# Optimization experiments

Hardware: AMD Instinct MI355X
Metric: run time of the kernel (lower is better)

## Reference

```python
import jax, jax.numpy as jnp
import numpy as np

LN_EPS = 1e-5
KERNEL_EPS = 1e-6


def setup_inputs() -> dict:
    key = jax.random.key(0)
    kx, kw, kb = jax.random.split(key, 3)
    B, N, D, H = 8, 2048, 256, 4
    x = jax.random.normal(kx, (B, N, D), dtype=jnp.float32) * 0.05
    log_sigmas = jnp.zeros((H, 1, 1), dtype=jnp.float32)
    W = jax.random.normal(kw, (D, D), dtype=jnp.float32) * 0.05  # torch Linear weight (out, in)
    b = jax.random.normal(kb, (D,), dtype=jnp.float32) * 0.05
    gamma = jnp.ones((D,), dtype=jnp.float32)
    beta = jnp.zeros((D,), dtype=jnp.float32)
    return {"x": x, "log_sigmas": log_sigmas, "W": W, "b": b, "gamma": gamma, "beta": beta}


def _layer_norm(y, gamma, beta):
    mu = jnp.mean(y, axis=-1, keepdims=True)
    var = jnp.var(y, axis=-1, keepdims=True)
    return (y - mu) * jax.lax.rsqrt(var + LN_EPS) * gamma + beta


def reference(x, log_sigmas, W, b, gamma, beta):
    # pairwise squared euclidean distances: (B, N, N)
    sq = jnp.sum(x * x, axis=-1)
    dist_sq = sq[:, :, None] + sq[:, None, :] - 2.0 * jnp.einsum('bnd,bmd->bnm', x, x)
    dist_sq = jnp.maximum(dist_sq, 0.0)
    # per-head Gaussian kernel adjacency, mean over heads
    sigmas = jnp.exp(log_sigmas)                      # (H,1,1)
    denom = 2.0 * sigmas ** 2 + KERNEL_EPS            # (H,1,1)
    adjs = jnp.exp(-dist_sq[:, None] / denom[None])   # (B,H,N,N)
    adj_final = jnp.mean(adjs, axis=1)                # (B,N,N)
    # aggregate, project, activate, residual layernorm
    out = jnp.einsum('bnm,bmd->bnd', adj_final, x)
    out = out @ W.T + b
    res = _layer_norm(jax.nn.elu(out) + x, gamma, beta)
    return res
```

## Files before the change

### kernel.cpp

```cpp
#include <hip/hip_runtime.h>

typedef unsigned short u16;
typedef __attribute__((ext_vector_type(8))) short bf16x8;
typedef __attribute__((ext_vector_type(4))) float f32x4;
typedef __attribute__((ext_vector_type(8))) unsigned short u16x8;

#define DEVI static __device__ __forceinline__

constexpr int Bb = 8, Nn = 2048, Dd = 256;

DEVI u16 f2bf(float f) {
    unsigned int u = __builtin_bit_cast(unsigned int, f);
    u = (u + 0x7fffu + ((u >> 16) & 1u)) >> 16;
    return (u16)u;
}
DEVI float bf2f(u16 v) {
    return __builtin_bit_cast(float, (unsigned int)v << 16);
}

DEVI void gl_lds16(const void* g, void* l) {
    __builtin_amdgcn_global_load_lds(
        (const __attribute__((address_space(1))) unsigned int*)g,
        (__attribute__((address_space(3))) unsigned int*)l, 16, 0, 0);
}

__global__ __launch_bounds__(256) void prep_xt_kernel(
    const float* __restrict__ x, u16* __restrict__ xb, u16* __restrict__ xbt,
    float* __restrict__ sq) {
    int n0 = blockIdx.x * 64;
    int b = blockIdx.y;
    int t = threadIdx.x;
    __shared__ __align__(16) u16 tile[64 * 256];
    int row = t >> 2;
    int c0 = (t & 3) * 64;
    const float* xr = x + ((size_t)(b * Nn + n0 + row)) * Dd + c0;
    u16* xbr = xb + ((size_t)(b * Nn + n0 + row)) * Dd + c0;
    float ss = 0.f;
#pragma unroll
    for (int cc = 0; cc < 16; ++cc) {
        float4 v = *(const float4*)(xr + cc * 4);
        ss += v.x * v.x + v.y * v.y + v.z * v.z + v.w * v.w;
        ushort4 o;
        o.x = f2bf(v.x); o.y = f2bf(v.y); o.z = f2bf(v.z); o.w = f2bf(v.w);
        *(ushort4*)(xbr + cc * 4) = o;
        int cb = (c0 + cc * 4) * 2;
        *(ushort4*)((char*)tile + row * 512 + (cb ^ ((row & 7) << 4))) = o;
    }
    ss += __shfl_xor(ss, 1);
    ss += __shfl_xor(ss, 2);
    if ((t & 3) == 0) sq[b * Nn + n0 + row] = ss;
    __syncthreads();
#pragma unroll
    for (int p = 0; p < 8; ++p) {
        int d = p * 32 + (t >> 3);
        int n8 = (t & 7) * 8;
        u16x8 vv;
#pragma unroll
        for (int e = 0; e < 8; ++e) {
            int r2 = n8 + e;
            vv[e] = *(const u16*)((char*)tile + r2 * 512 + ((d * 2) ^ ((r2 & 7) << 4)));
        }
        *(u16x8*)(xbt + ((size_t)(b * Dd + d)) * Nn + n0 + n8) = vv;
    }
}

__global__ void prep_w_kernel(const float* __restrict__ W, u16* __restrict__ Wb) {
    int i = (blockIdx.x * 256 + threadIdx.x) * 4;
    const float4 v = *(const float4*)(W + i);
    ushort4 o;
    o.x = f2bf(v.x); o.y = f2bf(v.y); o.z = f2bf(v.z); o.w = f2bf(v.w);
    *(ushort4*)(Wb + i) = o;
}

__global__ __launch_bounds__(256, 1) void fused_adj_kernel(
    const u16* __restrict__ xb, const u16* __restrict__ xbt,
    const float* __restrict__ sq, const float* __restrict__ lsig,
    u16* __restrict__ opart) {
    int bid = blockIdx.x;
    int xcd = bid & 7, j = bid >> 3;
    int g = xcd + 8 * (j >> 3);
    int nt8 = j & 7;
    int b = g >> 2, q = g & 3;
    int r0 = b * Nn + nt8 * 256;
    int m0b = b * Nn + q * 512;
    int mq0 = q * 512;

    int tid = threadIdx.x;
    int w = tid >> 6, l = tid & 63;
    int l15 = l & 15, lhi = l >> 4;

    __shared__ __align__(16) char smem[83968];
    char* sXmA = smem;
    char* sXmB = smem + 16384;
    char* sXmtA = smem + 32768;
    char* sXmtB = smem + 49152;
    char* sP = smem + 65536 + w * 4096;
    float* sq_lds = (float*)(smem + 81920);

    float nc[4];
#pragma unroll
    for (int h = 0; h < 4; ++h) {
        float denom = 2.f * expf(2.f * lsig[h]) + 1e-6f;
        nc[h] = -1.44269504f / denom;
    }
    bool uniform = (lsig[0] == lsig[1]) && (lsig[1] == lsig[2]) && (lsig[2] == lsig[3]);

    {
        int i2 = tid * 2;
        float2 v = *(const float2*)(sq + m0b + i2);
        *(float2*)(sq_lds + i2) = v;
    }

    bf16x8 bf[4][8];
    float sqn[4];
#pragma unroll
    for (int rg = 0; rg < 4; ++rg) {
        const u16* xr = xb + (size_t)(r0 + w * 64 + rg * 16 + l15) * Dd;
#pragma unroll
        for (int kt = 0; kt < 8; ++kt) bf[rg][kt] = *(const bf16x8*)(xr + kt * 32 + lhi * 8);
        sqn[rg] = sq[r0 + w * 64 + rg * 16 + l15];
    }

    f32x4 of[4][16];
#pragma unroll
    for (int rg = 0; rg < 4; ++rg)
#pragma unroll
        for (int dt = 0; dt < 16; ++dt) of[rg][dt] = (f32x4){0.f, 0.f, 0.f, 0.f};

    int swz = (l15 & 7) << 4;

#define STAGE(SXM, SXMT, tt) {                                                 \
    int m0_ = m0b + (tt) * 32;                                                 \
    int mc0_ = mq0 + (tt) * 32;                                                \
    _Pragma("unroll") for (int it = 0; it < 4; ++it) {                         \
        int c = w * 4 + it;                                                    \
        int row = c * 2 + (l >> 5);                                            \
        int col = l & 31;                                                      \
        gl_lds16(xb + (size_t)(m0_ + row) * Dd + (col ^ (row & 7)) * 8,        \
                 (SXM) + c * 1024);                                            \
    }                                                                           \
    _Pragma("unroll") for (int it = 0; it < 4; ++it) {                         \
        int c = w * 4 + it;                                                    \
        int drow = c * 16 + (l >> 2);                                          \
        gl_lds16(xbt + (size_t)(b * Dd + drow) * Nn + mc0_ + (l & 3) * 8,      \
                 (SXMT) + c * 1024);                                           \
    } }

#define COMPUTE(SXM, SXMT, tt) {                                               \
    _Pragma("unroll") for (int mt = 0; mt < 2; ++mt) {                         \
        float4 smv = *(const float4*)(sq_lds + (tt) * 32 + mt * 16 + lhi * 4); \
        f32x4 sfv[4];                                                          \
        _Pragma("unroll") for (int rg = 0; rg < 4; ++rg)                       \
            sfv[rg] = (f32x4){0.f, 0.f, 0.f, 0.f};                             \
        _Pragma("unroll") for (int kt = 0; kt < 8; ++kt) {                     \
            bf16x8 av = *(const bf16x8*)((SXM) + (mt * 16 + l15) * 512 +       \
                                         ((kt * 64 + lhi * 16) ^ swz));        \
            _Pragma("unroll") for (int rg = 0; rg < 4; ++rg)                   \
                sfv[rg] = __builtin_amdgcn_mfma_f32_16x16x32_bf16(             \
                    av, bf[rg][kt], sfv[rg], 0, 0, 0);                         \
        }                                                                       \
        float sm[4] = {smv.x, smv.y, smv.z, smv.w};                            \
        _Pragma("unroll") for (int rg = 0; rg < 4; ++rg) {                     \
            ushort4 pk;                                                        \
            _Pragma("unroll") for (int r = 0; r < 4; ++r) {                    \
                float d2 = fmaxf(fmaf(-2.f, sfv[rg][r], sqn[rg] + sm[r]), 0.f);\
                float p = exp2f(d2 * nc[0]);                                   \
                if (!uniform)                                                  \
                    p = 0.25f * (p + exp2f(d2 * nc[1]) + exp2f(d2 * nc[2]) +   \
                                 exp2f(d2 * nc[3]));                           \
                ((u16*)&pk)[r] = f2bf(p);                                      \
            }                                                                   \
            *(ushort4*)(sP + (rg * 16 + l15) * 64 + mt * 32 + lhi * 8) = pk;   \
        }                                                                       \
    }                                                                           \
    bf16x8 pa[4];                                                              \
    _Pragma("unroll") for (int rg = 0; rg < 4; ++rg)                           \
        pa[rg] = *(const bf16x8*)(sP + (rg * 16 + l15) * 64 + lhi * 16);       \
    _Pragma("unroll") for (int dt = 0; dt < 16; ++dt) {                        \
        bf16x8 bv = *(const bf16x8*)((SXMT) + (dt * 16 + l15) * 64 + lhi * 16);\
        _Pragma("unroll") for (int rg = 0; rg < 4; ++rg)                       \
            of[rg][dt] = __builtin_amdgcn_mfma_f32_16x16x32_bf16(              \
                pa[rg], bv, of[rg][dt], 0, 0, 0);                              \
    } }

    STAGE(sXmA, sXmtA, 0)
    __syncthreads();

    for (int tt = 0; tt < 8; ++tt) {
        int t0 = tt * 2;
        STAGE(sXmB, sXmtB, t0 + 1)
        asm volatile("s_waitcnt vmcnt(8)" ::: "memory");
        __builtin_amdgcn_s_barrier();
        COMPUTE(sXmA, sXmtA, t0)
        __builtin_amdgcn_s_barrier();
        if (tt < 7) {
            STAGE(sXmA, sXmtA, t0 + 2)
            asm volatile("s_waitcnt vmcnt(8)" ::: "memory");
        } else {
            asm volatile("s_waitcnt vmcnt(0)" ::: "memory");
        }
        __builtin_amdgcn_s_barrier();
        COMPUTE(sXmB, sXmtB, t0 + 1)
        __builtin_amdgcn_s_barrier();
    }

#undef STAGE
#undef COMPUTE

    u16* od = opart + (size_t)q * ((size_t)Bb * Nn * Dd);
#pragma unroll
    for (int rg = 0; rg < 4; ++rg)
#pragma unroll
        for (int dt = 0; dt < 16; ++dt)
#pragma unroll
            for (int r = 0; r < 4; ++r) {
                size_t row = (size_t)(r0 + w * 64 + rg * 16 + lhi * 4 + r);
                od[row * Dd + dt * 16 + l15] = f2bf(of[rg][dt][r]);
            }
}

__global__ __launch_bounds__(512, 1) void proj_ln_kernel(
    const u16* __restrict__ opart, const u16* __restrict__ Wb,
    const u16* __restrict__ xbres, const float* __restrict__ bvec,
    const float* __restrict__ gamma, const float* __restrict__ beta,
    float* __restrict__ out) {
    int tid = threadIdx.x, w = tid >> 6, l = tid & 63;
    int rg = w & 3, h = w >> 2;
    int lrow = l & 15, lhi = l >> 4;
    size_t row0 = (size_t)blockIdx.x * 64 + rg * 16;
    const size_t QS = (size_t)Bb * Nn * Dd;

    __shared__ __align__(16) float xch[8 * 16 * 2 * 64];

    f32x4 acc[16];
#pragma unroll
    for (int jt = 0; jt < 16; ++jt) acc[jt] = (f32x4){0.f, 0.f, 0.f, 0.f};

#pragma unroll
    for (int kk = 0; kk < 4; ++kk) {
        int kc = h * 4 + kk;
        float as[8] = {0.f, 0.f, 0.f, 0.f, 0.f, 0.f, 0.f, 0.f};
#pragma unroll
        for (int qq = 0; qq < 4; ++qq) {
            u16x8 v = *(const u16x8*)(opart + QS * qq + (row0 + lrow) * Dd + kc * 32 + lhi * 8);
#pragma unroll
            for (int e = 0; e < 8; ++e) as[e] += bf2f(v[e]);
        }
        bf16x8 a;
#pragma unroll
        for (int e = 0; e < 8; ++e) a[e] = (short)f2bf(as[e]);
#pragma unroll
        for (int jt = 0; jt < 16; ++jt) {
            bf16x8 bv = *(const bf16x8*)(Wb + (size_t)(jt * 16 + lrow) * Dd + kc * 32 + lhi * 8);
            acc[jt] = __builtin_amdgcn_mfma_f32_16x16x32_bf16(a, bv, acc[jt], 0, 0, 0);
        }
    }

#pragma unroll
    for (int jt = 0; jt < 16; ++jt)
#pragma unroll
        for (int qq = 0; qq < 2; ++qq) {
            int r = (1 - h) * 2 + qq;
            xch[(w * 16 + jt) * 128 + qq * 64 + l] = acc[jt][r];
        }
    __syncthreads();
#pragma unroll
    for (int jt = 0; jt < 16; ++jt)
#pragma unroll
        for (int qq = 0; qq < 2; ++qq)
            acc[jt][h * 2 + qq] += xch[((w ^ 4) * 16 + jt) * 128 + qq * 64 + l];

#pragma unroll
    for (int qq = 0; qq < 2; ++qq) {
        int r = h * 2 + qq;
        size_t grow = row0 + lhi * 4 + r;
        float vbuf[16];
        float s1 = 0.f, s2 = 0.f;
#pragma unroll
        for (int jt = 0; jt < 16; ++jt) {
            int jcol = jt * 16 + lrow;
            float v = acc[jt][r] + bvec[jcol];
            float e = v > 0.f ? v : (exp2f(v * 1.44269504f) - 1.f);
            float res = e + bf2f(xbres[grow * Dd + jcol]);
            vbuf[jt] = res;
            s1 += res;
            s2 += res * res;
        }
#pragma unroll
        for (int m = 1; m < 16; m <<= 1) {
            s1 += __shfl_xor(s1, m);
            s2 += __shfl_xor(s2, m);
        }
        float mean = s1 * (1.f / 256.f);
        float var = s2 * (1.f / 256.f) - mean * mean;
        float rstd = rsqrtf(var + 1e-5f);
#pragma unroll
        for (int jt = 0; jt < 16; ++jt) {
            int jcol = jt * 16 + lrow;
            out[grow * Dd + jcol] = (vbuf[jt] - mean) * rstd * gamma[jcol] + beta[jcol];
        }
    }
}

extern "C" void kernel_launch(void* const* d_in, const int* in_sizes, int n_in,
                              void* d_out, int out_size, void* d_ws, size_t ws_size,
                              hipStream_t stream) {
    const float* x = (const float*)d_in[0];
    const float* lsig = (const float*)d_in[1];
    const float* W = (const float*)d_in[2];
    const float* bvec = (const float*)d_in[3];
    const float* gamma = (const float*)d_in[4];
    const float* beta = (const float*)d_in[5];
    float* out = (float*)d_out;

    char* ws = (char*)d_ws;
    u16* xb = (u16*)ws;
    u16* xbt = (u16*)(ws + 8388608);
    float* sq = (float*)(ws + 16777216);
    u16* Wb = (u16*)(ws + 16842752);
    u16* opart = (u16*)(ws + 16973824);

    prep_xt_kernel<<<dim3(Nn / 64, Bb), dim3(256), 0, stream>>>(x, xb, xbt, sq);
    prep_w_kernel<<<dim3(64), dim3(256), 0, stream>>>(W, Wb);
    fused_adj_kernel<<<dim3(256), dim3(256), 0, stream>>>(xb, xbt, sq, lsig, opart);
    proj_ln_kernel<<<dim3(Bb * Nn / 64), dim3(512), 0, stream>>>(opart, Wb, xb, bvec, gamma, beta, out);
}
```

Measured before the change: 116.0 us.

## Restructure fused adjacency kernel to 8 waves with 64-wide m tiles and split PV

Moves the fused distance/exp/aggregate kernel to 512 threads and 64-column m tiles. Each wave now computes P for 32 rows, then cooperates on the P·X GEMM partitioned by 64-row and 128-column d blocks, with XOR-swizzled LDS for P and the transposed tile. The block-to-(batch, quarter) mapping changes, and s_setprio is placed around the MFMA sections. The aim is more waves to hide latency and fewer accumulators per wave. The cost is a larger LDS footprint, a single-buffered Xm tile with more barriers, and the loss of the XCD-aware block ordering.

```diff
diff --git a/kernel.cpp b/kernel.cpp
--- a/kernel.cpp
+++ b/kernel.cpp
@@ -72,15 +72,15 @@
     *(ushort4*)(Wb + i) = o;
 }
 
-__global__ __launch_bounds__(256, 1) void fused_adj_kernel(
+__global__ __launch_bounds__(512, 2) void fused_adj_kernel(
     const u16* __restrict__ xb, const u16* __restrict__ xbt,
     const float* __restrict__ sq, const float* __restrict__ lsig,
     u16* __restrict__ opart) {
     int bid = blockIdx.x;
-    int xcd = bid & 7, j = bid >> 3;
-    int g = xcd + 8 * (j >> 3);
-    int nt8 = j & 7;
-    int b = g >> 2, q = g & 3;
+    int b = bid & 7;
+    int j = bid >> 3;
+    int q = j & 3;
+    int nt8 = j >> 2;
     int r0 = b * Nn + nt8 * 256;
     int m0b = b * Nn + q * 512;
     int mq0 = q * 512;
@@ -88,14 +88,14 @@
     int tid = threadIdx.x;
     int w = tid >> 6, l = tid & 63;
     int l15 = l & 15, lhi = l >> 4;
-
-    __shared__ __align__(16) char smem[83968];
-    char* sXmA = smem;
-    char* sXmB = smem + 16384;
-    char* sXmtA = smem + 32768;
-    char* sXmtB = smem + 49152;
-    char* sP = smem + 65536 + w * 4096;
-    float* sq_lds = (float*)(smem + 81920);
+    int wn = w >> 1, wd = w & 1;
+
+    __shared__ __align__(16) char smem[133120];
+    char* sXm = smem;
+    char* xmtA = smem + 32768;
+    char* xmtB = smem + 65536;
+    char* sP = smem + 98304;
+    float* sq_lds = (float*)(smem + 131072);
 
     float nc[4];
 #pragma unroll
@@ -105,117 +105,123 @@
     }
     bool uniform = (lsig[0] == lsig[1]) && (lsig[1] == lsig[2]) && (lsig[2] == lsig[3]);
 
-    {
-        int i2 = tid * 2;
-        float2 v = *(const float2*)(sq + m0b + i2);
-        *(float2*)(sq_lds + i2) = v;
-    }
-
-    bf16x8 bf[4][8];
-    float sqn[4];
-#pragma unroll
-    for (int rg = 0; rg < 4; ++rg) {
-        const u16* xr = xb + (size_t)(r0 + w * 64 + rg * 16 + l15) * Dd;
+    sq_lds[tid] = sq[m0b + tid];
+
+    bf16x8 bf[2][8];
+    float sqn[2];
+#pragma unroll
+    for (int rg = 0; rg < 2; ++rg) {
+        const u16* xr = xb + (size_t)(r0 + w * 32 + rg * 16 + l15) * Dd;
 #pragma unroll
         for (int kt = 0; kt < 8; ++kt) bf[rg][kt] = *(const bf16x8*)(xr + kt * 32 + lhi * 8);
-        sqn[rg] = sq[r0 + w * 64 + rg * 16 + l15];
-    }
-
-    f32x4 of[4][16];
-#pragma unroll
-    for (int rg = 0; rg < 4; ++rg)
-#pragma unroll
-        for (int dt = 0; dt < 16; ++dt) of[rg][dt] = (f32x4){0.f, 0.f, 0.f, 0.f};
-
-    int swz = (l15 & 7) << 4;
-
-#define STAGE(SXM, SXMT, tt) {                                                 \
-    int m0_ = m0b + (tt) * 32;                                                 \
-    int mc0_ = mq0 + (tt) * 32;                                                \
+        sqn[rg] = sq[r0 + w * 32 + rg * 16 + l15];
+    }
+
+    f32x4 of[4][8];
+#pragma unroll
+    for (int ng = 0; ng < 4; ++ng)
+#pragma unroll
+        for (int dt = 0; dt < 8; ++dt) of[ng][dt] = (f32x4){0.f, 0.f, 0.f, 0.f};
+
+#define STAGE_XM(DST, tt) {                                                    \
     _Pragma("unroll") for (int it = 0; it < 4; ++it) {                         \
         int c = w * 4 + it;                                                    \
         int row = c * 2 + (l >> 5);                                            \
-        int col = l & 31;                                                      \
-        gl_lds16(xb + (size_t)(m0_ + row) * Dd + (col ^ (row & 7)) * 8,        \
-                 (SXM) + c * 1024);                                            \
-    }                                                                           \
+        gl_lds16(xb + (size_t)(m0b + (tt) * 64 + row) * Dd +                   \
+                     ((l & 31) ^ (row & 7)) * 8,                               \
+                 (DST) + c * 1024);                                            \
+    } }
+
+#define STAGE_XMT(DST, tt) {                                                   \
     _Pragma("unroll") for (int it = 0; it < 4; ++it) {                         \
         int c = w * 4 + it;                                                    \
-        int drow = c * 16 + (l >> 2);                                          \
-        gl_lds16(xbt + (size_t)(b * Dd + drow) * Nn + mc0_ + (l & 3) * 8,      \
-                 (SXMT) + c * 1024);                                           \
+        int d = c * 8 + (l >> 3);                                              \
+        gl_lds16(xbt + (size_t)(b * Dd + d) * Nn + mq0 + (tt) * 64 +           \
+                     ((l & 7) ^ (l >> 3)) * 8,                                 \
+                 (DST) + c * 1024);                                            \
     } }
 
-#define COMPUTE(SXM, SXMT, tt) {                                               \
-    _Pragma("unroll") for (int mt = 0; mt < 2; ++mt) {                         \
-        float4 smv = *(const float4*)(sq_lds + (tt) * 32 + mt * 16 + lhi * 4); \
-        f32x4 sfv[4];                                                          \
-        _Pragma("unroll") for (int rg = 0; rg < 4; ++rg)                       \
-            sfv[rg] = (f32x4){0.f, 0.f, 0.f, 0.f};                             \
+#define ITER(t, CUR, NXT, SN) {                                                \
+    if (SN) STAGE_XMT(NXT, (t) + 1)                                            \
+                            \
+    _Pragma("unroll") for (int mt = 0; mt < 4; ++mt) {                         \
+        float4 smv = *(const float4*)(sq_lds + (t) * 64 + mt * 16 + lhi * 4);  \
+        f32x4 sfv0 = (f32x4){0.f, 0.f, 0.f, 0.f};                              \
+        f32x4 sfv1 = (f32x4){0.f, 0.f, 0.f, 0.f};                              \
+        __builtin_amdgcn_s_setprio(1);                                         \
         _Pragma("unroll") for (int kt = 0; kt < 8; ++kt) {                     \
-            bf16x8 av = *(const bf16x8*)((SXM) + (mt * 16 + l15) * 512 +       \
-                                         ((kt * 64 + lhi * 16) ^ swz));        \
-            _Pragma("unroll") for (int rg = 0; rg < 4; ++rg)                   \
-                sfv[rg] = __builtin_amdgcn_mfma_f32_16x16x32_bf16(             \
-                    av, bf[rg][kt], sfv[rg], 0, 0, 0);                         \
+            bf16x8 av = *(const bf16x8*)(sXm + (mt * 16 + l15) * 512 +         \
+                                         ((kt * 64 + lhi * 16) ^ ((l15 & 7) << 4))); \
+            sfv0 = __builtin_amdgcn_mfma_f32_16x16x32_bf16(av, bf[0][kt], sfv0, 0, 0, 0); \
+            sfv1 = __builtin_amdgcn_mfma_f32_16x16x32_bf16(av, bf[1][kt], sfv1, 0, 0, 0); \
         }                                                                       \
+        __builtin_amdgcn_s_setprio(0);                                         \
         float sm[4] = {smv.x, smv.y, smv.z, smv.w};                            \
-        _Pragma("unroll") for (int rg = 0; rg < 4; ++rg) {                     \
+        _Pragma("unroll") for (int rg = 0; rg < 2; ++rg) {                     \
+            f32x4 sfv = rg ? sfv1 : sfv0;                                      \
             ushort4 pk;                                                        \
             _Pragma("unroll") for (int r = 0; r < 4; ++r) {                    \
-                float d2 = fmaxf(fmaf(-2.f, sfv[rg][r], sqn[rg] + sm[r]), 0.f);\
+                float d2 = fmaxf(fmaf(-2.f, sfv[r], sqn[rg] + sm[r]), 0.f);    \
                 float p = exp2f(d2 * nc[0]);                                   \
                 if (!uniform)                                                  \
                     p = 0.25f * (p + exp2f(d2 * nc[1]) + exp2f(d2 * nc[2]) +   \
                                  exp2f(d2 * nc[3]));                           \
                 ((u16*)&pk)[r] = f2bf(p);                                      \
             }                                                                   \
-            *(ushort4*)(sP + (rg * 16 + l15) * 64 + mt * 32 + lhi * 8) = pk;   \
+            int n_ = w * 32 + rg * 16 + l15;                                   \
+            *(ushort4*)(sP + n_ * 128 + ((mt * 32 + lhi * 8) ^ ((l15 & 7) << 4))) = pk; \
         }                                                                       \
     }                                                                           \
-    bf16x8 pa[4];                                                              \
-    _Pragma("unroll") for (int rg = 0; rg < 4; ++rg)                           \
-        pa[rg] = *(const bf16x8*)(sP + (rg * 16 + l15) * 64 + lhi * 16);       \
-    _Pragma("unroll") for (int dt = 0; dt < 16; ++dt) {                        \
-        bf16x8 bv = *(const bf16x8*)((SXMT) + (dt * 16 + l15) * 64 + lhi * 16);\
-        _Pragma("unroll") for (int rg = 0; rg < 4; ++rg)                       \
-            of[rg][dt] = __builtin_amdgcn_mfma_f32_16x16x32_bf16(              \
-                pa[rg], bv, of[rg][dt], 0, 0, 0);                              \
-    } }
-
-    STAGE(sXmA, sXmtA, 0)
+    asm volatile("s_waitcnt lgkmcnt(0)" ::: "memory");                         \
+    __builtin_amdgcn_s_barrier();                                              \
+    if (SN) STAGE_XM(sXm, (t) + 1)                                             \
+                            \
+    {                                                                           \
+        bf16x8 pa[4][2];                                                       \
+        _Pragma("unroll") for (int ng = 0; ng < 4; ++ng)                       \
+            _Pragma("unroll") for (int kt2 = 0; kt2 < 2; ++kt2) {              \
+                int n_ = wn * 64 + ng * 16 + l15;                              \
+                pa[ng][kt2] = *(const bf16x8*)(sP + n_ * 128 +                 \
+                    ((kt2 * 64 + lhi * 16) ^ ((l15 & 7) << 4)));               \
+            }                                                                   \
+        __builtin_amdgcn_s_setprio(1);                                         \
+        _Pragma("unroll") for (int dt = 0; dt < 8; ++dt) {                     \
+            _Pragma("unroll") for (int kt2 = 0; kt2 < 2; ++kt2) {              \
+                int d_ = wd * 128 + dt * 16 + l15;                             \
+                bf16x8 bv = *(const bf16x8*)((CUR) + d_ * 128 +                \
+                    ((kt2 * 64 + lhi * 16) ^ ((l15 & 7) << 4)));               \
+                _Pragma("unroll") for (int ng = 0; ng < 4; ++ng)               \
+                    of[ng][dt] = __builtin_amdgcn_mfma_f32_16x16x32_bf16(      \
+                        pa[ng][kt2], bv, of[ng][dt], 0, 0, 0);                 \
+            }                                                                   \
+        }                                                                       \
+        __builtin_amdgcn_s_setprio(0);                                         \
+    }                                                                           \
+    asm volatile("s_waitcnt vmcnt(0)" ::: "memory");                           \
+    __builtin_amdgcn_s_barrier(); }
+
+    STAGE_XM(sXm, 0)
+    STAGE_XMT(xmtA, 0)
     __syncthreads();
 
-    for (int tt = 0; tt < 8; ++tt) {
-        int t0 = tt * 2;
-        STAGE(sXmB, sXmtB, t0 + 1)
-        asm volatile("s_waitcnt vmcnt(8)" ::: "memory");
-        __builtin_amdgcn_s_barrier();
-        COMPUTE(sXmA, sXmtA, t0)
-        __builtin_amdgcn_s_barrier();
-        if (tt < 7) {
-            STAGE(sXmA, sXmtA, t0 + 2)
-            asm volatile("s_waitcnt vmcnt(8)" ::: "memory");
-        } else {
-            asm volatile("s_waitcnt vmcnt(0)" ::: "memory");
-        }
-        __builtin_amdgcn_s_barrier();
-        COMPUTE(sXmB, sXmtB, t0 + 1)
-        __builtin_amdgcn_s_barrier();
-    }
-
-#undef STAGE
-#undef COMPUTE
+    for (int tt = 0; tt < 4; ++tt) {
+        ITER(tt * 2, xmtA, xmtB, true)
+        ITER(tt * 2 + 1, xmtB, xmtA, (tt < 3))
+    }
+
+#undef STAGE_XM
+#undef STAGE_XMT
+#undef ITER
 
     u16* od = opart + (size_t)q * ((size_t)Bb * Nn * Dd);
 #pragma unroll
-    for (int rg = 0; rg < 4; ++rg)
-#pragma unroll
-        for (int dt = 0; dt < 16; ++dt)
+    for (int ng = 0; ng < 4; ++ng)
+#pragma unroll
+        for (int dt = 0; dt < 8; ++dt)
 #pragma unroll
             for (int r = 0; r < 4; ++r) {
-                size_t row = (size_t)(r0 + w * 64 + rg * 16 + lhi * 4 + r);
-                od[row * Dd + dt * 16 + l15] = f2bf(of[rg][dt][r]);
+                size_t row = (size_t)(r0 + wn * 64 + ng * 16 + lhi * 4 + r);
+                od[row * Dd + wd * 128 + dt * 16 + l15] = f2bf(of[ng][dt][r]);
             }
 }
 
@@ -322,6 +328,6 @@
 
     prep_xt_kernel<<<dim3(Nn / 64, Bb), dim3(256), 0, stream>>>(x, xb, xbt, sq);
     prep_w_kernel<<<dim3(64), dim3(256), 0, stream>>>(W, Wb);
-    fused_adj_kernel<<<dim3(256), dim3(256), 0, stream>>>(xb, xbt, sq, lsig, opart);
+    fused_adj_kernel<<<dim3(256), dim3(512), 0, stream>>>(xb, xbt, sq, lsig, opart);
     proj_ln_kernel<<<dim3(Bb * Nn / 64), dim3(512), 0, stream>>>(opart, Wb, xb, bvec, gamma, beta, out);
 }
```

After: 149.4 us. +28.7%, slower.
